# Optimization experiments

Hardware: AMD Instinct MI355X
Metric: run time of the kernel (lower is better)

## Reference

```python
import jax, jax.numpy as jnp
import numpy as np

C = 512
G = 4
CG = C // G            # 128 channels per group
R = max(1, CG // 8)    # 16 reduced dim per group
TOPK = max(1, int(C * 0.75))  # 384
TAU = 0.5
ALPHA = 0.1
EPS = 1e-8


def setup_inputs() -> dict:
    key = jax.random.key(0)
    k1, k2, k3, k4, k5, k6 = jax.random.split(key, 6)
    B, H, W = 16, 112, 112
    x = jax.random.normal(k1, (B, C, H, W), dtype=jnp.float32)
    noise_u = jax.random.uniform(k2, (B, C), dtype=jnp.float32)
    # grouped MLP params: Linear(2*CG -> R), ReLU, Linear(R -> CG), stacked over G
    W1 = jax.random.normal(k3, (G, 2 * CG, R), dtype=jnp.float32) * 0.05
    b1 = jax.random.normal(k4, (G, R), dtype=jnp.float32) * 0.05
    W2 = jax.random.normal(k5, (G, R, CG), dtype=jnp.float32) * 0.05
    b2 = jax.random.normal(k6, (G, CG), dtype=jnp.float32) * 0.05
    return {"x": x, "W1": W1, "b1": b1, "W2": W2, "b2": b2, "noise_u": noise_u}


def reference(x, W1, b1, W2, b2, noise_u):
    B = x.shape[0]
    # channel SE pooling: avg + max over HxW -> [B, C] each
    avg_pooled = jnp.mean(x, axis=(2, 3))
    max_pooled = jnp.max(x, axis=(2, 3))
    combined = jnp.concatenate([avg_pooled, max_pooled], axis=1)  # [B, 2C]
    # torch.chunk of the 2C vector into G groups (mixed avg/max slices)
    gf = combined.reshape(B, G, 2 * CG)  # [B, G, 2*CG]
    h = jax.nn.relu(jnp.einsum('bgi,gir->bgr', gf, W1) + b1)      # [B, G, R]
    score = (jnp.einsum('bgr,gro->bgo', h, W2) + b2).reshape(B, C)  # [B, C]
    # hard top-k mask
    _, topk_idx = jax.lax.top_k(score, TOPK)                      # [B, TOPK]
    hard_mask = jnp.zeros((B, C), dtype=score.dtype).at[
        jnp.arange(B)[:, None], topk_idx].set(1.0)
    # gumbel-sigmoid soft score (training branch)
    gumbel = -jnp.log(-jnp.log(noise_u + EPS) + EPS)
    soft = jax.nn.sigmoid((score + gumbel) / TAU)
    mask = hard_mask * soft                                        # [B, C]
    # residual blend: x*mask + x*(1-mask)*alpha
    blend = mask + (1.0 - mask) * ALPHA
    return x * blend[:, :, None, None]
```

## Files before the change

### kernel.cpp

```cpp
#include <hip/hip_runtime.h>
#include <math.h>

#define NC   512
#define NG   4
#define NCG  128
#define NR   16
#define NTOPK 384
#define NB   16
#define HW   (112 * 112)
#define NV4  (HW / 4)
#define ALPHA 0.1f
#define EPSC  1e-8f

typedef float f32x4 __attribute__((ext_vector_type(4)));

__global__ __launch_bounds__(256) void pool_kernel(
    const float* __restrict__ x, float* __restrict__ avg_out,
    float* __restrict__ max_out) {
  const int bc = blockIdx.x;
  const f32x4* p = reinterpret_cast<const f32x4*>(x + (size_t)bc * HW);
  float s = 0.f;
  float m = -INFINITY;
  for (int i = threadIdx.x; i < 3072; i += 1024) {
    f32x4 v0 = p[i];
    f32x4 v1 = p[i + 256];
    f32x4 v2 = p[i + 512];
    f32x4 v3 = p[i + 768];
    s += (v0.x + v0.y) + (v0.z + v0.w);
    s += (v1.x + v1.y) + (v1.z + v1.w);
    s += (v2.x + v2.y) + (v2.z + v2.w);
    s += (v3.x + v3.y) + (v3.z + v3.w);
    m = fmaxf(m, fmaxf(fmaxf(v0.x, v0.y), fmaxf(v0.z, v0.w)));
    m = fmaxf(m, fmaxf(fmaxf(v1.x, v1.y), fmaxf(v1.z, v1.w)));
    m = fmaxf(m, fmaxf(fmaxf(v2.x, v2.y), fmaxf(v2.z, v2.w)));
    m = fmaxf(m, fmaxf(fmaxf(v3.x, v3.y), fmaxf(v3.z, v3.w)));
  }
  if (threadIdx.x < 64) {
    f32x4 v = p[3072 + threadIdx.x];
    s += (v.x + v.y) + (v.z + v.w);
    m = fmaxf(m, fmaxf(fmaxf(v.x, v.y), fmaxf(v.z, v.w)));
  }
  #pragma unroll
  for (int off = 32; off > 0; off >>= 1) {
    s += __shfl_down(s, off, 64);
    m = fmaxf(m, __shfl_down(m, off, 64));
  }
  __shared__ float ss[4], sm[4];
  const int wave = threadIdx.x >> 6;
  const int lane = threadIdx.x & 63;
  if (lane == 0) { ss[wave] = s; sm[wave] = m; }
  __syncthreads();
  if (threadIdx.x == 0) {
    float st = (ss[0] + ss[1]) + (ss[2] + ss[3]);
    float mt = fmaxf(fmaxf(sm[0], sm[1]), fmaxf(sm[2], sm[3]));
    avg_out[bc] = st / (float)HW;
    max_out[bc] = mt;
  }
}

__global__ __launch_bounds__(512) void mask_kernel(
    const float* __restrict__ avg, const float* __restrict__ mx,
    const float* __restrict__ W1, const float* __restrict__ b1,
    const float* __restrict__ W2, const float* __restrict__ b2,
    const float* __restrict__ noise_u, float* __restrict__ blend) {
  const int b = blockIdx.x;
  const int t = threadIdx.x;
  __shared__ float comb[2 * NC];
  __shared__ float h[NG * NR];
  __shared__ float sc[NC];
  comb[t]      = avg[b * NC + t];
  comb[NC + t] = mx[b * NC + t];
  __syncthreads();
  if (t < NG * NR) {
    const int g = t / NR, r = t % NR;
    float acc = b1[g * NR + r];
    const float* w  = W1 + (size_t)g * (2 * NCG) * NR + r;
    const float* cf = comb + g * (2 * NCG);
    #pragma unroll 8
    for (int i = 0; i < 2 * NCG; ++i) acc += cf[i] * w[i * NR];
    h[t] = fmaxf(acc, 0.f);
  }
  __syncthreads();
  {
    const int g = t / NCG, o = t % NCG;
    float acc = b2[g * NCG + o];
    const float* w  = W2 + (size_t)g * NR * NCG + o;
    const float* hh = h + g * NR;
    #pragma unroll
    for (int r = 0; r < NR; ++r) acc += hh[r] * w[r * NCG];
    sc[t] = acc;
  }
  __syncthreads();
  const float my = sc[t];
  int cnt = 0;
  for (int j = 0; j < NC; ++j) {
    float v = sc[j];
    cnt += (v > my) || (v == my && j < t);
  }
  const float hard = (cnt < NTOPK) ? 1.f : 0.f;
  const float u = noise_u[b * NC + t];
  const float gum = -logf(-logf(u + EPSC) + EPSC);
  const float soft = 1.f / (1.f + expf(-(my + gum) * 2.0f));
  const float mask = hard * soft;
  blend[b * NC + t] = mask + (1.f - mask) * ALPHA;
}

__global__ __launch_bounds__(256) void scale_kernel(
    const float* __restrict__ x, const float* __restrict__ blend,
    float* __restrict__ out) {
  const int bc = (NB * NC - 1) - blockIdx.x;
  const float s = blend[bc];
  const f32x4* p = reinterpret_cast<const f32x4*>(x + (size_t)bc * HW);
  f32x4* q = reinterpret_cast<f32x4*>(out + (size_t)bc * HW);
  for (int i = threadIdx.x; i < 3072; i += 1024) {
    f32x4 v0 = p[i];
    f32x4 v1 = p[i + 256];
    f32x4 v2 = p[i + 512];
    f32x4 v3 = p[i + 768];
    v0 *= s; v1 *= s; v2 *= s; v3 *= s;
    __builtin_nontemporal_store(v0, &q[i]);
    __builtin_nontemporal_store(v1, &q[i + 256]);
    __builtin_nontemporal_store(v2, &q[i + 512]);
    __builtin_nontemporal_store(v3, &q[i + 768]);
  }
  if (threadIdx.x < 64) {
    const int i = 3072 + threadIdx.x;
    f32x4 v = p[i];
    v *= s;
    __builtin_nontemporal_store(v, &q[i]);
  }
}

extern "C" void kernel_launch(void* const* d_in, const int* in_sizes, int n_in,
                              void* d_out, int out_size, void* d_ws, size_t ws_size,
                              hipStream_t stream) {
  const float* x       = (const float*)d_in[0];
  const float* W1      = (const float*)d_in[1];
  const float* b1      = (const float*)d_in[2];
  const float* W2      = (const float*)d_in[3];
  const float* b2      = (const float*)d_in[4];
  const float* noise_u = (const float*)d_in[5];
  float* out = (float*)d_out;

  float* ws_avg   = (float*)d_ws;
  float* ws_max   = ws_avg + NB * NC;
  float* ws_blend = ws_max + NB * NC;

  pool_kernel<<<NB * NC, 256, 0, stream>>>(x, ws_avg, ws_max);
  mask_kernel<<<NB, 512, 0, stream>>>(ws_avg, ws_max, W1, b1, W2, b2,
                                      noise_u, ws_blend);
  scale_kernel<<<NB * NC, 256, 0, stream>>>(x, ws_blend, out);
}
```

Baseline: 230.7 us.

## Fuse mask computation into scale kernel, recomputing MLP per block

Merges the per-batch mask kernel and the scale kernel into one launch of 1024 blocks. Each block recomputes the small grouped MLP and scores for its batch, then ranks its own 8 channels with a split-and-shuffle count before scaling those 8 channel planes. This removes one kernel launch and the serialization behind a 16-block mask kernel, at the cost of redundant MLP work in every block and fewer, longer-running blocks in the streaming phase.

```diff
diff --git a/kernel.cpp b/kernel.cpp
--- a/kernel.cpp
+++ b/kernel.cpp
@@ -58,76 +58,110 @@
   }
 }
 
-__global__ __launch_bounds__(512) void mask_kernel(
-    const float* __restrict__ avg, const float* __restrict__ mx,
-    const float* __restrict__ W1, const float* __restrict__ b1,
-    const float* __restrict__ W2, const float* __restrict__ b2,
-    const float* __restrict__ noise_u, float* __restrict__ blend) {
-  const int b = blockIdx.x;
-  const int t = threadIdx.x;
+__global__ __launch_bounds__(256) void fused_kernel(
+    const float* __restrict__ x, const float* __restrict__ avg,
+    const float* __restrict__ mx, const float* __restrict__ W1,
+    const float* __restrict__ b1, const float* __restrict__ W2,
+    const float* __restrict__ b2, const float* __restrict__ noise_u,
+    float* __restrict__ out) {
+  const int rb = 1023 - (int)blockIdx.x;
+  const int b  = rb >> 6;
+  const int c0 = (rb & 63) * 8;
+  const int t  = threadIdx.x;
+
   __shared__ float comb[2 * NC];
   __shared__ float h[NG * NR];
   __shared__ float sc[NC];
-  comb[t]      = avg[b * NC + t];
-  comb[NC + t] = mx[b * NC + t];
-  __syncthreads();
-  if (t < NG * NR) {
-    const int g = t / NR, r = t % NR;
-    float acc = b1[g * NR + r];
-    const float* w  = W1 + (size_t)g * (2 * NCG) * NR + r;
-    const float* cf = comb + g * (2 * NCG);
-    #pragma unroll 8
-    for (int i = 0; i < 2 * NCG; ++i) acc += cf[i] * w[i * NR];
-    h[t] = fmaxf(acc, 0.f);
+  __shared__ float blend_loc[8];
+
+  {
+    const float* pa = avg + b * NC;
+    const float* pm = mx  + b * NC;
+    comb[t]             = pa[t];
+    comb[t + 256]       = pa[t + 256];
+    comb[512 + t]       = pm[t];
+    comb[512 + t + 256] = pm[t + 256];
   }
   __syncthreads();
+
   {
-    const int g = t / NCG, o = t % NCG;
+    const int pair = t >> 2, sub = t & 3;
+    const int g = pair >> 4, r = pair & 15;
+    const float* cf = comb + g * (2 * NCG);
+    const float* w  = W1 + (size_t)g * (2 * NCG) * NR + r;
+    const int i0 = sub * 64;
+    float acc = 0.f;
+    #pragma unroll 8
+    for (int i = 0; i < 64; ++i) acc += cf[i0 + i] * w[(i0 + i) * NR];
+    acc += __shfl_down(acc, 2, 4);
+    acc += __shfl_down(acc, 1, 4);
+    if (sub == 0) h[pair] = fmaxf(acc + b1[g * NR + r], 0.f);
+  }
+  __syncthreads();
+
+  #pragma unroll
+  for (int cc = 0; cc < 2; ++cc) {
+    const int c = t + cc * 256;
+    const int g = c >> 7, o = c & 127;
     float acc = b2[g * NCG + o];
     const float* w  = W2 + (size_t)g * NR * NCG + o;
     const float* hh = h + g * NR;
     #pragma unroll
     for (int r = 0; r < NR; ++r) acc += hh[r] * w[r * NCG];
-    sc[t] = acc;
+    sc[c] = acc;
   }
   __syncthreads();
-  const float my = sc[t];
-  int cnt = 0;
-  for (int j = 0; j < NC; ++j) {
-    float v = sc[j];
-    cnt += (v > my) || (v == my && j < t);
+
+  {
+    const int ci = t >> 5, sub = t & 31;
+    const int c = c0 + ci;
+    const float my = sc[c];
+    int cnt = 0;
+    const int j0 = sub * 16;
+    #pragma unroll
+    for (int jj = 0; jj < 16; ++jj) {
+      const int j = j0 + jj;
+      const float v = sc[j];
+      cnt += (v > my) || (v == my && j < c);
+    }
+    cnt += __shfl_down(cnt, 16, 32);
+    cnt += __shfl_down(cnt,  8, 32);
+    cnt += __shfl_down(cnt,  4, 32);
+    cnt += __shfl_down(cnt,  2, 32);
+    cnt += __shfl_down(cnt,  1, 32);
+    if (sub == 0) {
+      const float hard = (cnt < NTOPK) ? 1.f : 0.f;
+      const float u = noise_u[b * NC + c];
+      const float gum = -logf(-logf(u + EPSC) + EPSC);
+      const float soft = 1.f / (1.f + expf(-(my + gum) * 2.0f));
+      const float mask = hard * soft;
+      blend_loc[ci] = mask + (1.f - mask) * ALPHA;
+    }
   }
-  const float hard = (cnt < NTOPK) ? 1.f : 0.f;
-  const float u = noise_u[b * NC + t];
-  const float gum = -logf(-logf(u + EPSC) + EPSC);
-  const float soft = 1.f / (1.f + expf(-(my + gum) * 2.0f));
-  const float mask = hard * soft;
-  blend[b * NC + t] = mask + (1.f - mask) * ALPHA;
-}
+  __syncthreads();
 
-__global__ __launch_bounds__(256) void scale_kernel(
-    const float* __restrict__ x, const float* __restrict__ blend,
-    float* __restrict__ out) {
-  const int bc = (NB * NC - 1) - blockIdx.x;
-  const float s = blend[bc];
-  const f32x4* p = reinterpret_cast<const f32x4*>(x + (size_t)bc * HW);
-  f32x4* q = reinterpret_cast<f32x4*>(out + (size_t)bc * HW);
-  for (int i = threadIdx.x; i < 3072; i += 1024) {
-    f32x4 v0 = p[i];
-    f32x4 v1 = p[i + 256];
-    f32x4 v2 = p[i + 512];
-    f32x4 v3 = p[i + 768];
-    v0 *= s; v1 *= s; v2 *= s; v3 *= s;
-    __builtin_nontemporal_store(v0, &q[i]);
-    __builtin_nontemporal_store(v1, &q[i + 256]);
-    __builtin_nontemporal_store(v2, &q[i + 512]);
-    __builtin_nontemporal_store(v3, &q[i + 768]);
-  }
-  if (threadIdx.x < 64) {
-    const int i = 3072 + threadIdx.x;
-    f32x4 v = p[i];
-    v *= s;
-    __builtin_nontemporal_store(v, &q[i]);
+  for (int k = 7; k >= 0; --k) {
+    const int bc = rb * 8 + k;
+    const float s = blend_loc[k];
+    const f32x4* p = reinterpret_cast<const f32x4*>(x + (size_t)bc * HW);
+    f32x4* q = reinterpret_cast<f32x4*>(out + (size_t)bc * HW);
+    for (int i = t; i < 3072; i += 1024) {
+      f32x4 v0 = p[i];
+      f32x4 v1 = p[i + 256];
+      f32x4 v2 = p[i + 512];
+      f32x4 v3 = p[i + 768];
+      v0 *= s; v1 *= s; v2 *= s; v3 *= s;
+      __builtin_nontemporal_store(v0, &q[i]);
+      __builtin_nontemporal_store(v1, &q[i + 256]);
+      __builtin_nontemporal_store(v2, &q[i + 512]);
+      __builtin_nontemporal_store(v3, &q[i + 768]);
+    }
+    if (t < 64) {
+      const int i = 3072 + t;
+      f32x4 v = p[i];
+      v *= s;
+      __builtin_nontemporal_store(v, &q[i]);
+    }
   }
 }
 
@@ -142,12 +176,10 @@
   const float* noise_u = (const float*)d_in[5];
   float* out = (float*)d_out;
 
-  float* ws_avg   = (float*)d_ws;
-  float* ws_max   = ws_avg + NB * NC;
-  float* ws_blend = ws_max + NB * NC;
+  float* ws_avg = (float*)d_ws;
+  float* ws_max = ws_avg + NB * NC;
 
   pool_kernel<<<NB * NC, 256, 0, stream>>>(x, ws_avg, ws_max);
-  mask_kernel<<<NB, 512, 0, stream>>>(ws_avg, ws_max, W1, b1, W2, b2,
-                                      noise_u, ws_blend);
-  scale_kernel<<<NB * NC, 256, 0, stream>>>(x, ws_blend, out);
+  fused_kernel<<<1024, 256, 0, stream>>>(x, ws_avg, ws_max, W1, b1, W2, b2,
+                                         noise_u, out);
 }
```

Result: faster. 217.0 us (-5.9%).

## Process batch in chunks so scale pass rereads x from last-level cache

Applied to the files above, without the earlier changes.

Splits the pool/mask/scale pipeline into four batch chunks launched in sequence. Each chunk's slice of x is small enough to stay in the large last-level cache between the pooling read and the scaling read, cutting HBM traffic. The cost is more kernel launches and serialization bubbles around the tiny mask kernel. It also drops the previous reverse-order scale trick.

```diff
diff --git a/kernel.cpp b/kernel.cpp
--- a/kernel.cpp
+++ b/kernel.cpp
@@ -1,27 +1,31 @@
 #include <hip/hip_runtime.h>
 #include <math.h>
 
-#define NC   512
-#define NG   4
-#define NCG  128
-#define NR   16
+#define NC    512
+#define NG    4
+#define NCG   128
+#define NR    16
 #define NTOPK 384
-#define NB   16
-#define HW   (112 * 112)
-#define NV4  (HW / 4)
+#define NB    16
+#define HW    (112 * 112)
 #define ALPHA 0.1f
 #define EPSC  1e-8f
 
+#define CHUNK     4
+#define NCHUNK    (NB / CHUNK)
+#define BC_PER_CH (CHUNK * NC)
+
 typedef float f32x4 __attribute__((ext_vector_type(4)));
 
-__global__ __launch_bounds__(256) void pool_kernel(
+__global__ __launch_bounds__(256) void pool_chunk(
     const float* __restrict__ x, float* __restrict__ avg_out,
-    float* __restrict__ max_out) {
-  const int bc = blockIdx.x;
+    float* __restrict__ max_out, int ch) {
+  const int bc = ch * BC_PER_CH + (int)blockIdx.x;
+  const int t = threadIdx.x;
   const f32x4* p = reinterpret_cast<const f32x4*>(x + (size_t)bc * HW);
   float s = 0.f;
   float m = -INFINITY;
-  for (int i = threadIdx.x; i < 3072; i += 1024) {
+  for (int i = t; i < 3072; i += 1024) {
     f32x4 v0 = p[i];
     f32x4 v1 = p[i + 256];
     f32x4 v2 = p[i + 512];
@@ -35,8 +39,8 @@
     m = fmaxf(m, fmaxf(fmaxf(v2.x, v2.y), fmaxf(v2.z, v2.w)));
     m = fmaxf(m, fmaxf(fmaxf(v3.x, v3.y), fmaxf(v3.z, v3.w)));
   }
-  if (threadIdx.x < 64) {
-    f32x4 v = p[3072 + threadIdx.x];
+  if (t < 64) {
+    f32x4 v = p[3072 + t];
     s += (v.x + v.y) + (v.z + v.w);
     m = fmaxf(m, fmaxf(fmaxf(v.x, v.y), fmaxf(v.z, v.w)));
   }
@@ -46,11 +50,10 @@
     m = fmaxf(m, __shfl_down(m, off, 64));
   }
   __shared__ float ss[4], sm[4];
-  const int wave = threadIdx.x >> 6;
-  const int lane = threadIdx.x & 63;
+  const int wave = t >> 6, lane = t & 63;
   if (lane == 0) { ss[wave] = s; sm[wave] = m; }
   __syncthreads();
-  if (threadIdx.x == 0) {
+  if (t == 0) {
     float st = (ss[0] + ss[1]) + (ss[2] + ss[3]);
     float mt = fmaxf(fmaxf(sm[0], sm[1]), fmaxf(sm[2], sm[3]));
     avg_out[bc] = st / (float)HW;
@@ -58,12 +61,12 @@
   }
 }
 
-__global__ __launch_bounds__(512) void mask_kernel(
+__global__ __launch_bounds__(512) void mask_chunk(
     const float* __restrict__ avg, const float* __restrict__ mx,
     const float* __restrict__ W1, const float* __restrict__ b1,
     const float* __restrict__ W2, const float* __restrict__ b2,
-    const float* __restrict__ noise_u, float* __restrict__ blend) {
-  const int b = blockIdx.x;
+    const float* __restrict__ noise_u, float* __restrict__ blend, int ch) {
+  const int b = ch * CHUNK + (int)blockIdx.x;
   const int t = threadIdx.x;
   __shared__ float comb[2 * NC];
   __shared__ float h[NG * NR];
@@ -105,14 +108,15 @@
   blend[b * NC + t] = mask + (1.f - mask) * ALPHA;
 }
 
-__global__ __launch_bounds__(256) void scale_kernel(
+__global__ __launch_bounds__(256) void scale_chunk(
     const float* __restrict__ x, const float* __restrict__ blend,
-    float* __restrict__ out) {
-  const int bc = (NB * NC - 1) - blockIdx.x;
+    float* __restrict__ out, int ch) {
+  const int bc = ch * BC_PER_CH + (int)blockIdx.x;
+  const int t = threadIdx.x;
   const float s = blend[bc];
   const f32x4* p = reinterpret_cast<const f32x4*>(x + (size_t)bc * HW);
   f32x4* q = reinterpret_cast<f32x4*>(out + (size_t)bc * HW);
-  for (int i = threadIdx.x; i < 3072; i += 1024) {
+  for (int i = t; i < 3072; i += 1024) {
     f32x4 v0 = p[i];
     f32x4 v1 = p[i + 256];
     f32x4 v2 = p[i + 512];
@@ -123,8 +127,8 @@
     __builtin_nontemporal_store(v2, &q[i + 512]);
     __builtin_nontemporal_store(v3, &q[i + 768]);
   }
-  if (threadIdx.x < 64) {
-    const int i = 3072 + threadIdx.x;
+  if (t < 64) {
+    const int i = 3072 + t;
     f32x4 v = p[i];
     v *= s;
     __builtin_nontemporal_store(v, &q[i]);
@@ -146,8 +150,10 @@
   float* ws_max   = ws_avg + NB * NC;
   float* ws_blend = ws_max + NB * NC;
 
-  pool_kernel<<<NB * NC, 256, 0, stream>>>(x, ws_avg, ws_max);
-  mask_kernel<<<NB, 512, 0, stream>>>(ws_avg, ws_max, W1, b1, W2, b2,
-                                      noise_u, ws_blend);
-  scale_kernel<<<NB * NC, 256, 0, stream>>>(x, ws_blend, out);
+  for (int ch = 0; ch < NCHUNK; ++ch) {
+    pool_chunk<<<BC_PER_CH, 256, 0, stream>>>(x, ws_avg, ws_max, ch);
+    mask_chunk<<<CHUNK, 512, 0, stream>>>(ws_avg, ws_max, W1, b1, W2, b2,
+                                          noise_u, ws_blend, ch);
+    scale_chunk<<<BC_PER_CH, 256, 0, stream>>>(x, ws_blend, out, ch);
+  }
 }
```

New measurement: 306.1 us. +32.6%, slower.
